# Kernel tuning notes

Hardware: AMD Instinct MI355X
Metric: run time of the kernel (lower is better)

## Reference

```python
import jax, jax.numpy as jnp
import numpy as np

V = 25000
E = 100000
NODE_IN = 74
EDGE_IN = 12
OUT = 64
EHID = 128
NUM_STEPS = 6


def setup_inputs() -> dict:
    key = jax.random.key(0)
    ks = jax.random.split(key, 12)
    s = 0.05
    node_feats = jax.random.normal(ks[0], (V, NODE_IN), dtype=jnp.float32)
    edge_feats = jax.random.normal(ks[1], (E, EDGE_IN), dtype=jnp.float32)
    src = jax.random.randint(ks[2], (E,), 0, V)
    dst = jax.random.randint(ks[3], (E,), 0, V)
    # project_node_feats: Linear(node_in, out)
    Wp = jax.random.normal(ks[4], (NODE_IN, OUT), dtype=jnp.float32) * s
    bp = jnp.zeros((OUT,), dtype=jnp.float32)
    # edge network: Linear(edge_in, ehid) -> ReLU -> Linear(ehid, out*out)
    We1 = jax.random.normal(ks[5], (EDGE_IN, EHID), dtype=jnp.float32) * s
    be1 = jnp.zeros((EHID,), dtype=jnp.float32)
    We2 = jax.random.normal(ks[6], (EHID, OUT * OUT), dtype=jnp.float32) * s
    be2 = jnp.zeros((OUT * OUT,), dtype=jnp.float32)
    # NNConv output bias
    bias = jnp.zeros((OUT,), dtype=jnp.float32)
    return {
        "node_feats": node_feats, "edge_feats": edge_feats,
        "src": src, "dst": dst,
        "Wp": Wp, "bp": bp,
        "We1": We1, "be1": be1, "We2": We2, "be2": be2,
        "bias": bias,
    }


def reference(node_feats, edge_feats, src, dst, Wp, bp, We1, be1, We2, be2, bias):
    # project node features
    h = jax.nn.relu(node_feats @ Wp + bp)  # [V, OUT]
    # per-edge weight matrices (same every step -> hoist out of loop)
    ew = jax.nn.relu(edge_feats @ We1 + be1) @ We2 + be2  # [E, OUT*OUT]
    ew = ew.reshape(E, OUT, OUT)
    for _ in range(NUM_STEPS):
        # gather src node feats, batched matvec, scatter-sum to dst
        msg = jnp.einsum('ei,eio->eo', h[src], ew)  # [E, OUT]
        agg = jax.ops.segment_sum(msg, dst, num_segments=V)  # [V, OUT]
        h = jax.nn.relu(agg + bias)
    return h
```

## Files before the change

### kernel.cpp

```cpp
#include <hip/hip_runtime.h>
#include <hip/hip_bf16.h>

#define Vn 25000
#define En 100000
#define NODE_IN 74
#define EDGE_IN 12
#define OUTD 64
#define EHID 128
#define NUM_STEPS 6

typedef __attribute__((ext_vector_type(8))) _Float16 half8;
typedef __attribute__((ext_vector_type(2))) _Float16 half2v;
typedef __attribute__((ext_vector_type(4))) float floatx4;

__global__ void proj_kernel(const float* __restrict__ node,
                            const float* __restrict__ Wp,
                            const float* __restrict__ bp,
                            float* __restrict__ h) {
  __shared__ float nf[NODE_IN];
  int v = blockIdx.x;
  int o = threadIdx.x;
  for (int i = o; i < NODE_IN; i += 64) nf[i] = node[(size_t)v * NODE_IN + i];
  __syncthreads();
  float acc = bp[o];
  for (int i = 0; i < NODE_IN; ++i) acc = fmaf(nf[i], Wp[i * OUTD + o], acc);
  h[(size_t)v * OUTD + o] = fmaxf(acc, 0.0f);
}

__global__ void edge_kernel(const float* __restrict__ ef,
                            const float* __restrict__ We1,
                            const float* __restrict__ be1,
                            _Float16* __restrict__ f) {
  __shared__ float es[EDGE_IN];
  int e = blockIdx.x;
  int k = threadIdx.x;
  if (k < EDGE_IN) es[k] = ef[(size_t)e * EDGE_IN + k];
  __syncthreads();
  float acc = be1[k];
  for (int j = 0; j < EDGE_IN; ++j) acc = fmaf(es[j], We1[j * EHID + k], acc);
  f[(size_t)e * EHID + k] = (_Float16)fmaxf(acc, 0.0f);
}

__global__ void w2r_kernel(const float* __restrict__ We2,
                           _Float16* __restrict__ w2s) {
  int g = blockIdx.x * 256 + threadIdx.x;
  int j = g & 7;
  int quad = (g >> 3) & 3;
  int l15 = (g >> 5) & 15;
  int c = (g >> 9) & 3;
  int step = g >> 11;
  int s = step & 3;
  int i = step >> 2;
  int k = s * 32 + quad * 8 + j;
  int col = i * 64 + c * 16 + l15;
  int eidx = g & 2047;
  int estore = eidx ^ (((eidx >> 6) & 3) << 3);
  w2s[((size_t)step << 11) | estore] = (_Float16)We2[(size_t)k * (OUTD * OUTD) + col];
}

#define GLOAD_LDS(gp, lp)                                                     \
  __builtin_amdgcn_global_load_lds(                                           \
      (const __attribute__((address_space(1))) void*)(gp),                    \
      (__attribute__((address_space(3))) void*)(lp), 16, 0, 0)

__global__ __launch_bounds__(256, 3) void msg_kernel(
    const float* __restrict__ h,
    const _Float16* __restrict__ f,
    const _Float16* __restrict__ w2s,
    const int* __restrict__ src,
    const int* __restrict__ dst,
    const float* __restrict__ be2,
    float* __restrict__ agg) {
  __shared__ __align__(16) char smem_raw[32768];
  __shared__ int s_dst[128];

  const int tid = threadIdx.x;
  const int wv = tid >> 6;
  const int lane = tid & 63;
  const int quad = lane >> 4;
  const int l15 = lane & 15;
  const int e0 = blockIdx.x * 128;
  const int ew0 = e0 + wv * 32;

  _Float16* h16w = (_Float16*)(smem_raw + wv * 4096);
  char* ring = smem_raw + 16384;

  if (lane < 32) {
    int eg = ew0 + lane;
    s_dst[wv * 32 + lane] = (eg < En) ? dst[eg] : -1;
  }
  {
    int el = lane & 31;
    int ih = lane >> 5;
    int eg = ew0 + el;
    int sv = (eg < En) ? src[eg] : 0;
    const float4* hp = reinterpret_cast<const float4*>(h + (size_t)sv * OUTD + ih * 32);
    int pe = (el & 15) * 2 + (el >> 4);
#pragma unroll
    for (int c = 0; c < 8; ++c) {
      float4 v = hp[c];
      int i4 = ih * 32 + c * 4;
      h16w[(i4 + 0) * 32 + pe] = (_Float16)v.x;
      h16w[(i4 + 1) * 32 + pe] = (_Float16)v.y;
      h16w[(i4 + 2) * 32 + pe] = (_Float16)v.z;
      h16w[(i4 + 3) * 32 + pe] = (_Float16)v.w;
    }
  }

  half8 afr[2][4];
#pragma unroll
  for (int t = 0; t < 2; ++t) {
    int e = ew0 + t * 16 + l15;
    if (e >= En) e = En - 1;
    const _Float16* fr = f + (size_t)e * EHID + quad * 8;
#pragma unroll
    for (int s = 0; s < 4; ++s)
      afr[t][s] = *reinterpret_cast<const half8*>(fr + s * 32);
  }

  floatx4 acc[2][4];
  const floatx4 zero4 = (floatx4){0.f, 0.f, 0.f, 0.f};
#pragma unroll
  for (int t = 0; t < 2; ++t)
#pragma unroll
    for (int c = 0; c < 4; ++c) acc[t][c] = zero4;

  const char* w2b = (const char*)w2s;
  const int roff = l15 * 64 + ((quad ^ ((l15 >> 1) & 3)) << 4);
  const char* sp0 = ring + roff;
  const char* sp1 = ring + 4096 + roff;
  const char* sp2 = ring + 8192 + roff;
  const char* sp3 = ring + 12288 + roff;

#define STAGE1(GS, SLOT)                                                      \
  {                                                                           \
    const char* gp_ = w2b + (size_t)(GS) * 4096 + (wv << 10) + lane * 16;     \
    char* lp_ = ring + (SLOT) * 4096 + (wv << 10);                            \
    GLOAD_LDS(gp_, lp_);                                                      \
  }

  asm volatile("s_waitcnt vmcnt(0)" ::: "memory");

  STAGE1(0, 0);
  STAGE1(1, 1);
  STAGE1(2, 2);

  half2v hv = *reinterpret_cast<const half2v*>(h16w + l15 * 2);
  half2v hvn;

#define KSTEP(SS, SPS, GST)                                                   \
  {                                                                           \
    asm volatile("s_waitcnt vmcnt(2)" ::: "memory");                          \
    asm volatile("s_barrier" ::: "memory");                                   \
    half8 B0 = *reinterpret_cast<const half8*>(SPS);                          \
    half8 B1 = *reinterpret_cast<const half8*>(SPS + 1024);                   \
    half8 B2 = *reinterpret_cast<const half8*>(SPS + 2048);                   \
    half8 B3 = *reinterpret_cast<const half8*>(SPS + 3072);                   \
    int gs_ = (GST) > 255 ? 255 : (GST);                                      \
    STAGE1(gs_, ((SS) + 3) & 3);                                              \
    __builtin_amdgcn_s_setprio(1);                                            \
    _Pragma("unroll") for (int t = 0; t < 2; ++t) {                           \
      half8 as = afr[t][SS] * hb[t];                                          \
      acc[t][0] = __builtin_amdgcn_mfma_f32_16x16x32_f16(as, B0, acc[t][0], 0, 0, 0); \
      acc[t][1] = __builtin_amdgcn_mfma_f32_16x16x32_f16(as, B1, acc[t][1], 0, 0, 0); \
      acc[t][2] = __builtin_amdgcn_mfma_f32_16x16x32_f16(as, B2, acc[t][2], 0, 0, 0); \
      acc[t][3] = __builtin_amdgcn_mfma_f32_16x16x32_f16(as, B3, acc[t][3], 0, 0, 0); \
    }                                                                         \
    __builtin_amdgcn_s_setprio(0);                                            \
  }

  for (int i = 0; i < 64; ++i) {
    half8 hb[2];
#pragma unroll
    for (int t = 0; t < 2; ++t) {
      _Float16 hf = hv[t];
      hb[t] = (half8){hf, hf, hf, hf, hf, hf, hf, hf};
    }
    int gs = i * 4;
    KSTEP(0, sp0, gs + 3);
    {
      int inx = (i < 63) ? i + 1 : 63;
      hvn = *reinterpret_cast<const half2v*>(h16w + inx * 32 + l15 * 2);
    }
    KSTEP(1, sp1, gs + 4);
    KSTEP(2, sp2, gs + 5);
    KSTEP(3, sp3, gs + 6);
    hv = hvn;
  }

  asm volatile("s_waitcnt vmcnt(0)" ::: "memory");

  {
#pragma unroll
    for (int s = 0; s < 2; ++s) {
      half8 b2f[4];
#pragma unroll
      for (int c = 0; c < 4; ++c) {
        half8 v;
#pragma unroll
        for (int j = 0; j < 8; ++j)
          v[j] = (_Float16)be2[(s * 32 + quad * 8 + j) * 64 + c * 16 + l15];
        b2f[c] = v;
      }
#pragma unroll
      for (int t = 0; t < 2; ++t) {
        half8 ha;
#pragma unroll
        for (int j = 0; j < 8; ++j)
          ha[j] = h16w[(s * 32 + quad * 8 + j) * 32 + l15 * 2 + t];
#pragma unroll
        for (int c = 0; c < 4; ++c)
          acc[t][c] = __builtin_amdgcn_mfma_f32_16x16x32_f16(ha, b2f[c], acc[t][c], 0, 0, 0);
      }
    }
  }

#pragma unroll
  for (int t = 0; t < 2; ++t) {
    int rb = wv * 32 + t * 16 + quad * 4;
#pragma unroll
    for (int c = 0; c < 4; ++c) {
      int col = c * 16 + l15;
#pragma unroll
      for (int r = 0; r < 4; ++r) {
        int d = s_dst[rb + r];
        if (d >= 0) atomicAdd(&agg[(size_t)d * OUTD + col], acc[t][c][r]);
      }
    }
  }
}

__global__ void update_kernel(float* __restrict__ agg,
                              const float* __restrict__ bias,
                              float* __restrict__ hout,
                              float* __restrict__ dout, int last) {
  int g = blockIdx.x * 256 + threadIdx.x;
  if (g >= Vn * OUTD) return;
  float v = agg[g];
  agg[g] = 0.0f;
  float r = fmaxf(v + bias[g & 63], 0.0f);
  hout[g] = r;
  if (last) dout[g] = r;
}

extern "C" void kernel_launch(void* const* d_in, const int* in_sizes, int n_in,
                              void* d_out, int out_size, void* d_ws, size_t ws_size,
                              hipStream_t stream) {
  const float* node = (const float*)d_in[0];
  const float* edge = (const float*)d_in[1];
  const int* src = (const int*)d_in[2];
  const int* dst = (const int*)d_in[3];
  const float* Wp   = (const float*)d_in[4];
  const float* bp   = (const float*)d_in[5];
  const float* We1  = (const float*)d_in[6];
  const float* be1  = (const float*)d_in[7];
  const float* We2  = (const float*)d_in[8];
  const float* be2  = (const float*)d_in[9];
  const float* bias = (const float*)d_in[10];
  float* out = (float*)d_out;

  char* ws = (char*)d_ws;
  float* agg = (float*)(ws);
  float* h_a = (float*)(ws + 6400000);
  float* h_b = (float*)(ws + 12800000);
  _Float16* f   = (_Float16*)(ws + 19200000);
  _Float16* w2s = (_Float16*)(ws + 44800000);

  hipMemsetAsync(agg, 0, (size_t)Vn * OUTD * sizeof(float), stream);
  proj_kernel<<<Vn, 64, 0, stream>>>(node, Wp, bp, h_a);
  edge_kernel<<<En, 128, 0, stream>>>(edge, We1, be1, f);
  w2r_kernel<<<(OUTD * OUTD * EHID) / 256, 256, 0, stream>>>(We2, w2s);

  float* hin = h_a;
  float* hout = h_b;
  const int nblocks = (En + 127) / 128;
  for (int s = 0; s < NUM_STEPS; ++s) {
    msg_kernel<<<nblocks, 256, 0, stream>>>(hin, f, w2s, src, dst, be2, agg);
    update_kernel<<<(Vn * OUTD + 255) / 256, 256, 0, stream>>>(
        agg, bias, hout, out, s == NUM_STEPS - 1);
    float* t = hin; hin = hout; hout = t;
  }
}
```

Before: 820.6 us.

## Deepen LDS weight ring to eight slots and double-buffer B fragments in registers

The shared-memory ring holding the streamed per-edge weight tiles grows from four to eight 4 KB slots, with seven stages prefetched up front. The main loop is unrolled by two so the B fragments for the next k-step are read from LDS into registers while the MFMAs consume the current set (P/Q ping-pong). The aim is to hide global-to-LDS latency and LDS read latency behind the MFMA work. In exchange LDS per block rises to about 48 KB and register pressure goes up, which may limit occupancy. The per-step wait stays at vmcnt(2), so the extra prefetch depth may be only partly used.

```diff
diff --git a/kernel.cpp b/kernel.cpp
--- a/kernel.cpp
+++ b/kernel.cpp
@@ -71,7 +71,7 @@
     const int* __restrict__ dst,
     const float* __restrict__ be2,
     float* __restrict__ agg) {
-  __shared__ __align__(16) char smem_raw[32768];
+  __shared__ __align__(16) char smem_raw[49152];
   __shared__ int s_dst[128];
 
   const int tid = threadIdx.x;
@@ -131,6 +131,10 @@
   const char* sp1 = ring + 4096 + roff;
   const char* sp2 = ring + 8192 + roff;
   const char* sp3 = ring + 12288 + roff;
+  const char* sp4 = ring + 16384 + roff;
+  const char* sp5 = ring + 20480 + roff;
+  const char* sp6 = ring + 24576 + roff;
+  const char* sp7 = ring + 28672 + roff;
 
 #define STAGE1(GS, SLOT)                                                      \
   {                                                                           \
@@ -144,48 +148,66 @@
   STAGE1(0, 0);
   STAGE1(1, 1);
   STAGE1(2, 2);
+  STAGE1(3, 3);
+  STAGE1(4, 4);
+  STAGE1(5, 5);
+  STAGE1(6, 6);
+  asm volatile("s_waitcnt vmcnt(6)" ::: "memory");
+  asm volatile("s_barrier" ::: "memory");
+  half8 P[4], Q[4];
+  P[0] = *reinterpret_cast<const half8*>(sp0);
+  P[1] = *reinterpret_cast<const half8*>(sp0 + 1024);
+  P[2] = *reinterpret_cast<const half8*>(sp0 + 2048);
+  P[3] = *reinterpret_cast<const half8*>(sp0 + 3072);
 
   half2v hv = *reinterpret_cast<const half2v*>(h16w + l15 * 2);
   half2v hvn;
 
-#define KSTEP(SS, SPS, GST)                                                   \
+#define KSTEP(SS, BMM, BRD, SPRD, STSL, GST)                                  \
   {                                                                           \
     asm volatile("s_waitcnt vmcnt(2)" ::: "memory");                          \
     asm volatile("s_barrier" ::: "memory");                                   \
-    half8 B0 = *reinterpret_cast<const half8*>(SPS);                          \
-    half8 B1 = *reinterpret_cast<const half8*>(SPS + 1024);                   \
-    half8 B2 = *reinterpret_cast<const half8*>(SPS + 2048);                   \
-    half8 B3 = *reinterpret_cast<const half8*>(SPS + 3072);                   \
+    BRD[0] = *reinterpret_cast<const half8*>(SPRD);                           \
+    BRD[1] = *reinterpret_cast<const half8*>(SPRD + 1024);                    \
+    BRD[2] = *reinterpret_cast<const half8*>(SPRD + 2048);                    \
+    BRD[3] = *reinterpret_cast<const half8*>(SPRD + 3072);                    \
     int gs_ = (GST) > 255 ? 255 : (GST);                                      \
-    STAGE1(gs_, ((SS) + 3) & 3);                                              \
+    STAGE1(gs_, STSL);                                                        \
     __builtin_amdgcn_s_setprio(1);                                            \
     _Pragma("unroll") for (int t = 0; t < 2; ++t) {                           \
       half8 as = afr[t][SS] * hb[t];                                          \
-      acc[t][0] = __builtin_amdgcn_mfma_f32_16x16x32_f16(as, B0, acc[t][0], 0, 0, 0); \
-      acc[t][1] = __builtin_amdgcn_mfma_f32_16x16x32_f16(as, B1, acc[t][1], 0, 0, 0); \
-      acc[t][2] = __builtin_amdgcn_mfma_f32_16x16x32_f16(as, B2, acc[t][2], 0, 0, 0); \
-      acc[t][3] = __builtin_amdgcn_mfma_f32_16x16x32_f16(as, B3, acc[t][3], 0, 0, 0); \
+      acc[t][0] = __builtin_amdgcn_mfma_f32_16x16x32_f16(as, BMM[0], acc[t][0], 0, 0, 0); \
+      acc[t][1] = __builtin_amdgcn_mfma_f32_16x16x32_f16(as, BMM[1], acc[t][1], 0, 0, 0); \
+      acc[t][2] = __builtin_amdgcn_mfma_f32_16x16x32_f16(as, BMM[2], acc[t][2], 0, 0, 0); \
+      acc[t][3] = __builtin_amdgcn_mfma_f32_16x16x32_f16(as, BMM[3], acc[t][3], 0, 0, 0); \
     }                                                                         \
     __builtin_amdgcn_s_setprio(0);                                            \
   }
 
-  for (int i = 0; i < 64; ++i) {
+#define BUILD_HB(HSRC)                                                        \
+  _Pragma("unroll") for (int t = 0; t < 2; ++t) {                             \
+    _Float16 hf = (HSRC)[t];                                                  \
+    hb[t] = (half8){hf, hf, hf, hf, hf, hf, hf, hf};                          \
+  }
+
+  for (int ip = 0; ip < 32; ++ip) {
+    int g = ip * 8;
     half8 hb[2];
-#pragma unroll
-    for (int t = 0; t < 2; ++t) {
-      _Float16 hf = hv[t];
-      hb[t] = (half8){hf, hf, hf, hf, hf, hf, hf, hf};
+    BUILD_HB(hv);
+    KSTEP(0, P, Q, sp1, 7, g + 7);
+    hvn = *reinterpret_cast<const half2v*>(h16w + (2 * ip + 1) * 32 + l15 * 2);
+    KSTEP(1, Q, P, sp2, 0, g + 8);
+    KSTEP(2, P, Q, sp3, 1, g + 9);
+    KSTEP(3, Q, P, sp4, 2, g + 10);
+    BUILD_HB(hvn);
+    KSTEP(0, P, Q, sp5, 3, g + 11);
+    {
+      int inx = (ip < 31) ? 2 * ip + 2 : 63;
+      hv = *reinterpret_cast<const half2v*>(h16w + inx * 32 + l15 * 2);
     }
-    int gs = i * 4;
-    KSTEP(0, sp0, gs + 3);
-    {
-      int inx = (i < 63) ? i + 1 : 63;
-      hvn = *reinterpret_cast<const half2v*>(h16w + inx * 32 + l15 * 2);
-    }
-    KSTEP(1, sp1, gs + 4);
-    KSTEP(2, sp2, gs + 5);
-    KSTEP(3, sp3, gs + 6);
-    hv = hvn;
+    KSTEP(1, Q, P, sp6, 4, g + 12);
+    KSTEP(2, P, Q, sp7, 5, g + 13);
+    KSTEP(3, Q, P, sp0, 6, g + 14);
   }
 
   asm volatile("s_waitcnt vmcnt(0)" ::: "memory");
```

Result: slower. 940.2 us (+14.6%).
